# Kernel tuning notes

Hardware: AMD Instinct MI355X
Metric: run time of the kernel (lower is better)

The kernel has to match this reference:

```python
import jax, jax.numpy as jnp
import numpy as np
from jax import lax

EPS = 1e-5

def _silu(x):
    return x * jax.nn.sigmoid(x)

def _mamba_seq(x, ln_w, ln_b, in_w, conv_w, conv_b, xp_w, dt_w, dt_b, A_log, Dp, out_w):
    # x: [B, L, dim] token sequence
    di = conv_w.shape[0]          # d_inner
    ds = A_log.shape[1]           # d_state
    dtr = dt_w.shape[1]           # dt_rank
    kw = conv_w.shape[2]          # d_conv
    # LayerNorm
    mu = jnp.mean(x, axis=-1, keepdims=True)
    var = jnp.mean((x - mu) ** 2, axis=-1, keepdims=True)
    xn = (x - mu) * lax.rsqrt(var + EPS) * ln_w + ln_b
    # in_proj -> (x, z)
    xz = xn @ in_w.T                       # [B,L,2*di]
    xs, z = xz[..., :di], xz[..., di:]
    # causal depthwise conv1d over L
    xc = lax.conv_general_dilated(xs.transpose(0, 2, 1), conv_w, (1,),
                                  [(kw - 1, 0)], feature_group_count=di,
                                  dimension_numbers=('NCH', 'OIH', 'NCH'))
    xc = _silu(xc + conv_b[None, :, None]).transpose(0, 2, 1)   # [B,L,di]
    # x_proj -> dt, B, C
    dbc = xc @ xp_w.T                      # [B,L,dtr+2*ds]
    dt = jax.nn.softplus(dbc[..., :dtr] @ dt_w.T + dt_b)        # [B,L,di]
    Bm = dbc[..., dtr:dtr + ds]            # [B,L,ds]
    Cm = dbc[..., dtr + ds:]               # [B,L,ds]
    A = -jnp.exp(A_log)                    # [di,ds]
    dA = jnp.exp(dt[..., None] * A)        # [B,L,di,ds]
    dBu = (dt * xc)[..., None] * Bm[:, :, None, :]              # [B,L,di,ds]
    # selective scan: h_t = dA_t * h_{t-1} + dBu_t (parallel associative scan)
    def comb(e1, e2):
        a1, b1 = e1
        a2, b2 = e2
        return a1 * a2, a2 * b1 + b2
    _, h = lax.associative_scan(comb, (dA, dBu), axis=1)
    y = jnp.einsum('blds,bls->bld', h, Cm) + xc * Dp
    return (y * _silu(z)) @ out_w.T

def _mamba_block(x5, *p):
    # x5: [B,C,D,H,W] -> flatten spatial dims to tokens
    B, C = x5.shape[:2]
    xf = x5.reshape(B, C, -1).transpose(0, 2, 1)   # [B,L,C]
    y = _mamba_seq(xf, *p)
    return y.transpose(0, 2, 1).reshape(x5.shape)

def _conv3d(x, w, b):
    return lax.conv_general_dilated(x, w, (1, 1, 1), [(1, 1)] * 3,
                                    dimension_numbers=('NCDHW', 'OIDHW', 'NCDHW')) \
           + b[None, :, None, None, None]

def _bn3d(x, g, b):
    # BatchNorm3d in training mode: batch statistics over (B,D,H,W)
    m = jnp.mean(x, axis=(0, 2, 3, 4), keepdims=True)
    v = jnp.mean((x - m) ** 2, axis=(0, 2, 3, 4), keepdims=True)
    return (x - m) * lax.rsqrt(v + EPS) * g.reshape(1, -1, 1, 1, 1) + b.reshape(1, -1, 1, 1, 1)

def _mamba_params(key, dim, d_state=16, d_conv=4, expand=2):
    di = expand * dim
    dtr = max(1, -(-dim // 16))
    ks = jax.random.split(key, 5)
    return {
        'ln_w': jnp.ones((dim,), jnp.float32),
        'ln_b': jnp.zeros((dim,), jnp.float32),
        'in_w': jax.random.normal(ks[0], (2 * di, dim), jnp.float32) * (dim ** -0.5),
        'conv_w': jax.random.normal(ks[1], (di, 1, d_conv), jnp.float32) * 0.3,
        'conv_b': jnp.zeros((di,), jnp.float32),
        'xp_w': jax.random.normal(ks[2], (dtr + 2 * d_state, di), jnp.float32) * (di ** -0.5),
        'dt_w': jax.random.normal(ks[3], (di, dtr), jnp.float32) * (dtr ** -0.5),
        'dt_b': jnp.log(jnp.expm1(jnp.full((di,), 0.01, jnp.float32))),
        'A_log': jnp.log(jnp.tile(jnp.arange(1, d_state + 1, dtype=jnp.float32)[None, :], (di, 1))),
        'D': jnp.ones((di,), jnp.float32),
        'out_w': jax.random.normal(ks[4], (dim, di), jnp.float32) * (di ** -0.5),
    }

def setup_inputs() -> dict:
    key = jax.random.key(0)
    k = jax.random.split(key, 8)
    inp = {
        'l': jax.random.normal(k[0], (1, 16, 16, 48, 48), jnp.float32),
        's': jax.random.normal(k[1], (1, 16, 16, 48, 48), jnp.float32),
    }
    for name, p in _mamba_params(k[2], 32).items():
        inp['m1_' + name] = p
    for name, p in _mamba_params(k[3], 16).items():
        inp['m2_' + name] = p
    inp['c1_w'] = jax.random.normal(k[4], (16, 32, 3, 3, 3), jnp.float32) * ((32 * 27) ** -0.5)
    inp['c1_b'] = jnp.zeros((16,), jnp.float32)
    inp['bn1_g'] = jnp.ones((16,), jnp.float32)
    inp['bn1_b'] = jnp.zeros((16,), jnp.float32)
    inp['c2_w'] = jax.random.normal(k[5], (16, 16, 3, 3, 3), jnp.float32) * ((16 * 27) ** -0.5)
    inp['c2_b'] = jnp.zeros((16,), jnp.float32)
    inp['bn2_g'] = jnp.ones((16,), jnp.float32)
    inp['bn2_b'] = jnp.zeros((16,), jnp.float32)
    return inp

def reference(l, s,
              m1_ln_w, m1_ln_b, m1_in_w, m1_conv_w, m1_conv_b, m1_xp_w, m1_dt_w, m1_dt_b, m1_A_log, m1_D, m1_out_w,
              m2_ln_w, m2_ln_b, m2_in_w, m2_conv_w, m2_conv_b, m2_xp_w, m2_dt_w, m2_dt_b, m2_A_log, m2_D, m2_out_w,
              c1_w, c1_b, bn1_g, bn1_b, c2_w, c2_b, bn2_g, bn2_b):
    x = jnp.concatenate([l, s], axis=1)                         # [B,32,D,H,W]
    x = _mamba_block(x, m1_ln_w, m1_ln_b, m1_in_w, m1_conv_w, m1_conv_b,
                     m1_xp_w, m1_dt_w, m1_dt_b, m1_A_log, m1_D, m1_out_w) + x
    x = _bn3d(_conv3d(x, c1_w, c1_b), bn1_g, bn1_b)             # [B,16,D,H,W]
    x = _mamba_block(x, m2_ln_w, m2_ln_b, m2_in_w, m2_conv_w, m2_conv_b,
                     m2_xp_w, m2_dt_w, m2_dt_b, m2_A_log, m2_D, m2_out_w) + x
    x = _bn3d(_conv3d(x, c2_w, c2_b), bn2_g, bn2_b)
    return x
```

## Files before the change

### kernel.cpp

```cpp
#include <hip/hip_runtime.h>
#include <math.h>

#define L_TOT 36864
#define BN_EPS 1e-5f
#define PCH 45000

typedef __attribute__((ext_vector_type(8))) short bf16x8;
typedef __attribute__((ext_vector_type(4))) float f32x4;

__device__ __forceinline__ float fsigmoid(float x){ return 1.f/(1.f+__expf(-x)); }
__device__ __forceinline__ float fsoftplus(float x){
  float e = __expf(x);
  return (x>20.f)? x : __logf(1.f+e);
}
__device__ __forceinline__ unsigned short f2bf(float x){
  union { float f; unsigned u; } cv; cv.f = x;
  unsigned r = (cv.u + 0x7FFFu + ((cv.u>>16)&1u)) >> 16;
  return (unsigned short)r;
}
__host__ __device__ constexpr int off3c(int r){
  return (r>=27) ? 0 : ((r/9)-1)*2500 + (((r%9)/3)-1)*50 + ((r%3)-1);
}

template<int DIM, int DI, int DTR, bool DOBN, bool SETUP>
__global__ __launch_bounds__(256) void k_front(
    const float* __restrict__ x0, const float* __restrict__ x1,
    const float* __restrict__ bstats, const float* __restrict__ bg, const float* __restrict__ bbp,
    const float* __restrict__ lnw, const float* __restrict__ lnb,
    const float* __restrict__ inw,
    const float* __restrict__ cw, const float* __restrict__ cb,
    const float* __restrict__ xpw,
    const float* __restrict__ dtw, const float* __restrict__ dtb,
    const float* __restrict__ Alog,
    float* __restrict__ xcg, float* __restrict__ zg,
    float* __restrict__ dtpg, float* __restrict__ Bg, float* __restrict__ Cg,
    float* __restrict__ aggA, float* __restrict__ aggB,
    const float* __restrict__ cvw1, unsigned short* __restrict__ wA1,
    const float* __restrict__ cvw2, unsigned short* __restrict__ wA2,
    float* __restrict__ stats, float* __restrict__ bfz)
{
  constexpr int TCH  = 48;
  constexpr int ROWS = DTR + 32;
  constexpr int NSH  = 256/DI;
  constexpr int SPB  = 16/NSH;
  constexpr int CH   = DI*16;
  constexpr int R0SZ = DI*64;
  constexpr int O_SXC = R0SZ;
  constexpr int O_SB  = O_SXC + DI*49;
  constexpr int O_SC  = O_SB + 16*49;
  constexpr int O_DTP = O_SC + 16*49;
  constexpr int SMEM  = O_DTP + DTR*48 + 64;
  __shared__ float sm[SMEM];

  const int tid   = threadIdx.x;
  const int chunk = blockIdx.x;
  const int t0    = chunk*TCH;

  if constexpr (SETUP){
    for (int idx = blockIdx.x*256 + tid; idx < 16*PCH; idx += 768*256)
      bfz[idx] = 0.f;
    const int b = blockIdx.x;
    if (b < 4){
      int k = b*256 + tid;
      if (k < 864){
        int ic = k & 31, r = k >> 5;
        for (int m=0;m<16;m++){
          float v = (r < 27) ? cvw1[m*32*27 + ic*27 + r] : 0.f;
          wA1[(((k>>3)*16) + m)*8 + (k&7)] = f2bf(v);
        }
      }
    } else if (b < 6){
      int k = (b-4)*256 + tid;
      if (k < 448){
        int ic = k & 15, r = k >> 4;
        for (int m=0;m<16;m++){
          float v = (r < 27) ? cvw2[m*16*27 + ic*27 + r] : 0.f;
          wA2[(((k>>3)*16) + m)*8 + (k&7)] = f2bf(v);
        }
      }
    } else if (b == 6){
      if (tid < 64) stats[tid] = 0.f;
    }
  }

  for (int idx = tid; idx < DIM*64; idx += 256){
    int c = idx >> 6, i2 = idx & 63;
    int t = t0 - 3 + i2;
    float v = 0.f;
    if (i2 < 51 && t >= 0){
      if constexpr (DOBN){
        float raw = x0[c*L_TOT + t];
        float bm = bstats[2*c]*(1.f/L_TOT);
        float bv = bstats[2*c+1]*(1.f/L_TOT) - bm*bm;
        v = (raw - bm)*rsqrtf(bv+BN_EPS)*bg[c] + bbp[c];
      } else {
        v = (c < 16) ? x0[c*L_TOT + t] : x1[(c-16)*L_TOT + t];
      }
    }
    sm[idx] = v;
  }
  __syncthreads();

  if (tid < 64){
    float s = 0.f, s2 = 0.f;
#pragma unroll
    for (int c = 0; c < DIM; c++){
      float v = sm[c*64 + tid];
      s += v; s2 += v*v;
    }
    float m  = s*(1.f/DIM);
    float var = s2*(1.f/DIM) - m*m;
    float rs = rsqrtf(var + BN_EPS);
#pragma unroll
    for (int c = 0; c < DIM; c++){
      float v = sm[c*64 + tid];
      sm[c*64 + tid] = (v-m)*rs*lnw[c] + lnb[c];
    }
  }
  __syncthreads();

  const int i   = tid & 63;
  const int r0w = __builtin_amdgcn_readfirstlane(tid >> 6);
  {
    float xn[DIM];
#pragma unroll
    for (int c = 0; c < DIM; c++) xn[c] = sm[c*64 + i];
    __syncthreads();
    for (int r = r0w; r < 2*DI; r += 4){
      float acc = 0.f;
#pragma unroll
      for (int c = 0; c < DIM; c++) acc += xn[c]*inw[r*DIM + c];
      if (r < DI){
        if (i < 51) sm[r*64 + i] = (t0 == 0 && i < 3) ? 0.f : acc;
      } else {
        if (i >= 3 && i < 51) zg[(r-DI)*L_TOT + t0 + i - 3] = acc;
      }
    }
  }
  __syncthreads();

  for (int idx = tid; idx < DI*48; idx += 256){
    int d = idx / 48, j = idx - d*48;
    const float* xr = &sm[d*64 + j];
    float acc = cb[d] + cw[d*4+0]*xr[0] + cw[d*4+1]*xr[1]
                      + cw[d*4+2]*xr[2] + cw[d*4+3]*xr[3];
    sm[O_SXC + d*49 + j] = acc * fsigmoid(acc);
  }
  __syncthreads();

  {
    constexpr int NR = (ROWS + 3) / 4;
    float acc[NR];
#pragma unroll
    for (int rr = 0; rr < NR; rr++) acc[rr] = 0.f;
    for (int db = 0; db < DI; db += 16){
      float xcol[16];
#pragma unroll
      for (int k = 0; k < 16; k++) xcol[k] = sm[O_SXC + (db+k)*49 + i];
#pragma unroll
      for (int rr = 0; rr < NR; rr++){
        int r = r0w + rr*4;
        if (r < ROWS){
          float a2 = 0.f;
#pragma unroll
          for (int k = 0; k < 16; k++) a2 += xcol[k]*xpw[r*DI + db + k];
          acc[rr] += a2;
        }
      }
    }
    if (i < 48){
#pragma unroll
      for (int rr = 0; rr < NR; rr++){
        int r = r0w + rr*4;
        if (r < ROWS){
          if (r < DTR)          sm[O_DTP + r*48 + i] = acc[rr];
          else if (r < DTR+16)  sm[O_SB + (r-DTR)*49 + i] = acc[rr];
          else                  sm[O_SC + (r-DTR-16)*49 + i] = acc[rr];
        }
      }
    }
  }
  __syncthreads();

  for (int idx = tid; idx < DI*48; idx += 256){
    int d = idx / 48, j = idx - d*48;
    float pre = dtb[d] + dtw[d*DTR]*sm[O_DTP + j];
    if (DTR > 1) pre += dtw[d*DTR + DTR-1]*sm[O_DTP + (DTR-1)*48 + j];
    sm[d*49 + j] = fsoftplus(pre);
  }
  __syncthreads();

  for (int idx = tid; idx < DI*12; idx += 256){
    int d = idx / 12, q = idx - d*12;
    float4 v = make_float4(sm[O_SXC + d*49 + q*4+0], sm[O_SXC + d*49 + q*4+1],
                           sm[O_SXC + d*49 + q*4+2], sm[O_SXC + d*49 + q*4+3]);
    *reinterpret_cast<float4*>(xcg + d*L_TOT + t0 + q*4) = v;
  }
  for (int idx = tid; idx < ROWS*12; idx += 256){
    int r = idx / 12, q = idx - r*12;
    const float* src; float* dst;
    if (r < DTR)        { src = &sm[O_DTP + r*48 + q*4];          dst = dtpg + r*L_TOT + t0 + q*4; }
    else if (r < DTR+16){ src = &sm[O_SB + (r-DTR)*49 + q*4];     dst = Bg + (r-DTR)*L_TOT + t0 + q*4; }
    else                { src = &sm[O_SC + (r-DTR-16)*49 + q*4];  dst = Cg + (r-DTR-16)*L_TOT + t0 + q*4; }
    *reinterpret_cast<float4*>(dst) = make_float4(src[0], src[1], src[2], src[3]);
  }

  {
    const int d  = tid / NSH;
    const int sh = tid - d*NSH;
    float Av[SPB], Ar[SPB], Br[SPB];
#pragma unroll
    for (int j = 0; j < SPB; j++){
      Av[j] = -__expf(Alog[d*16 + sh*SPB + j]);
      Ar[j] = 1.f; Br[j] = 0.f;
    }
    for (int t = 0; t < TCH; t++){
      float dtv = sm[d*49 + t];
      float bb2 = dtv * sm[O_SXC + d*49 + t];
#pragma unroll
      for (int j = 0; j < SPB; j++){
        float a2 = __expf(dtv*Av[j]);
        Ar[j] *= a2;
        Br[j] = a2*Br[j] + bb2*sm[O_SB + (sh*SPB+j)*49 + t];
      }
    }
    const int o = chunk*CH + tid*SPB;
    if constexpr (SPB == 4){
      *reinterpret_cast<float4*>(&aggA[o]) = make_float4(Ar[0],Ar[1],Ar[2],Ar[3]);
      *reinterpret_cast<float4*>(&aggB[o]) = make_float4(Br[0],Br[1],Br[2],Br[3]);
    } else {
      *reinterpret_cast<float2*>(&aggA[o]) = make_float2(Ar[0],Ar[1]);
      *reinterpret_cast<float2*>(&aggB[o]) = make_float2(Br[0],Br[1]);
    }
  }
}

template<int NCH>
__global__ __launch_bounds__(256) void k_carry(const float* __restrict__ aggA,
                        const float* __restrict__ aggB,
                        float* __restrict__ carry, int CH) {
  constexpr int SEG = NCH/16;
  const int chl = threadIdx.x & 15;
  const int seg = threadIdx.x >> 4;
  const int ch  = blockIdx.x*16 + chl;
  const int c0  = seg*SEG;
  float a = 1.f, b = 0.f;
  for (int cb=c0; cb<c0+SEG; cb+=8){
    float av[8], bv[8];
#pragma unroll
    for (int k=0;k<8;k++){ av[k]=aggA[(cb+k)*CH+ch]; bv[k]=aggB[(cb+k)*CH+ch]; }
#pragma unroll
    for (int k=0;k<8;k++){ a = a*av[k]; b = av[k]*b + bv[k]; }
  }
  __shared__ float sa[16][17], sb[16][17];
  sa[seg][chl]=a; sb[seg][chl]=b;
  __syncthreads();
  if (threadIdx.x < 16){
    float pa=1.f, pb=0.f;
    for (int g=0; g<16; g++){
      float ca=sa[g][threadIdx.x], cb2=sb[g][threadIdx.x];
      sa[g][threadIdx.x]=pa; sb[g][threadIdx.x]=pb;
      float na = pa*ca;
      float nb = ca*pb + cb2;
      pa=na; pb=nb;
    }
  }
  __syncthreads();
  float h = sb[seg][chl];
  for (int cb=c0; cb<c0+SEG; cb+=8){
    float av[8], bv[8];
#pragma unroll
    for (int k=0;k<8;k++){ av[k]=aggA[(cb+k)*CH+ch]; bv[k]=aggB[(cb+k)*CH+ch]; }
#pragma unroll
    for (int k=0;k<8;k++){ carry[(cb+k)*CH+ch]=h; h = av[k]*h + bv[k]; }
  }
}

template<int DIM, int DI, int DTR, int RES>
__global__ __launch_bounds__(256) void k_back(
    const float* __restrict__ xcg, const float* __restrict__ zg,
    const float* __restrict__ dtpg, const float* __restrict__ Bg, const float* __restrict__ Cg,
    const float* __restrict__ dtw, const float* __restrict__ dtb,
    const float* __restrict__ Alog, const float* __restrict__ Dp,
    const float* __restrict__ carry,
    const float* __restrict__ ow,
    const float* __restrict__ r0src, const float* __restrict__ r1src,
    const float* __restrict__ bstats, const float* __restrict__ bg, const float* __restrict__ bbp,
    unsigned short* __restrict__ rp)
{
  constexpr int TCH = 48;
  constexpr int NSH = 256/DI;
  constexpr int SPB = 16/NSH;
  constexpr int ROWS = DTR + 32;
  constexpr int O_SXC = 0;
  constexpr int O_SDT = O_SXC + DI*49;
  constexpr int O_SB  = O_SDT + DI*49;
  constexpr int O_SC  = O_SB + 16*49;
  constexpr int O_SY  = O_SC + 16*49;
  constexpr int O_DTP = O_SY + DI*49;
  constexpr int SMEM  = O_DTP + DTR*48 + 64;
  __shared__ float sm[SMEM];
  const int tid   = threadIdx.x;
  const int chunk = blockIdx.x;
  const int t0    = chunk*TCH;

  for (int idx = tid; idx < DI*12; idx += 256){
    int d = idx / 12, q = idx - d*12;
    float4 v = *reinterpret_cast<const float4*>(xcg + d*L_TOT + t0 + q*4);
    sm[O_SXC + d*49 + q*4+0] = v.x; sm[O_SXC + d*49 + q*4+1] = v.y;
    sm[O_SXC + d*49 + q*4+2] = v.z; sm[O_SXC + d*49 + q*4+3] = v.w;
  }
  for (int idx = tid; idx < ROWS*12; idx += 256){
    int r = idx / 12, q = idx - r*12;
    const float* src; float* dst;
    if (r < DTR)        { src = dtpg + r*L_TOT + t0 + q*4;         dst = &sm[O_DTP + r*48 + q*4]; }
    else if (r < DTR+16){ src = Bg + (r-DTR)*L_TOT + t0 + q*4;     dst = &sm[O_SB + (r-DTR)*49 + q*4]; }
    else                { src = Cg + (r-DTR-16)*L_TOT + t0 + q*4;  dst = &sm[O_SC + (r-DTR-16)*49 + q*4]; }
    float4 v = *reinterpret_cast<const float4*>(src);
    dst[0] = v.x; dst[1] = v.y; dst[2] = v.z; dst[3] = v.w;
  }
  __syncthreads();
  for (int idx = tid; idx < DI*48; idx += 256){
    int d = idx / 48, j = idx - d*48;
    float pre = dtb[d] + dtw[d*DTR]*sm[O_DTP + j];
    if (DTR > 1) pre += dtw[d*DTR + DTR-1]*sm[O_DTP + 48 + j];
    sm[O_SDT + d*49 + j] = fsoftplus(pre);
  }
  __syncthreads();

  {
    const int d  = tid / NSH;
    const int sh = tid - d*NSH;
    float Av[SPB], h[SPB];
#pragma unroll
    for (int j = 0; j < SPB; j++){
      Av[j] = -__expf(Alog[d*16 + sh*SPB + j]);
      h[j]  = carry[chunk*(DI*16) + tid*SPB + j];
    }
    const float Dv = Dp[d];
    for (int t = 0; t < TCH; t++){
      float dtv = sm[O_SDT + d*49 + t];
      float xcv = sm[O_SXC + d*49 + t];
      float bb2 = dtv*xcv;
      float p = 0.f;
#pragma unroll
      for (int j = 0; j < SPB; j++){
        float a2 = __expf(dtv*Av[j]);
        h[j] = a2*h[j] + bb2*sm[O_SB + (sh*SPB+j)*49 + t];
        p += h[j]*sm[O_SC + (sh*SPB+j)*49 + t];
      }
#pragma unroll
      for (int o = 1; o < NSH; o <<= 1) p += __shfl_xor(p, o);
      if (sh == 0) sm[O_SY + d*49 + t] = p + xcv*Dv;
    }
  }
  __syncthreads();
  for (int idx = tid; idx < DI*12; idx += 256){
    int d = idx / 12, q = idx - d*12;
    float4 zv = *reinterpret_cast<const float4*>(zg + d*L_TOT + t0 + q*4);
    sm[O_SY + d*49 + q*4+0] *= zv.x*fsigmoid(zv.x);
    sm[O_SY + d*49 + q*4+1] *= zv.y*fsigmoid(zv.y);
    sm[O_SY + d*49 + q*4+2] *= zv.z*fsigmoid(zv.z);
    sm[O_SY + d*49 + q*4+3] *= zv.w*fsigmoid(zv.w);
  }
  __syncthreads();

  {
    const int col = tid & 63;
    const int r0w = __builtin_amdgcn_readfirstlane(tid >> 6);
    constexpr int NO = DIM/4;
    float acc[NO];
#pragma unroll
    for (int rr = 0; rr < NO; rr++) acc[rr] = 0.f;
    for (int db = 0; db < DI; db += 16){
      float ycol[16];
#pragma unroll
      for (int k = 0; k < 16; k++) ycol[k] = sm[O_SY + (db+k)*49 + col];
#pragma unroll
      for (int rr = 0; rr < NO; rr++){
        int r = r0w + rr*4;
        float a2 = 0.f;
#pragma unroll
        for (int k = 0; k < 16; k++) a2 += ycol[k]*ow[r*DI + db + k];
        acc[rr] += a2;
      }
    }
    if (col < 48){
      const int t  = t0 + col;
      const int zz = chunk / 48, yy = chunk - zz*48;
      const int pb = (zz+1)*2500 + (yy+1)*50 + (col+1);
#pragma unroll
      for (int rr = 0; rr < NO; rr++){
        int r = r0w + rr*4;
        float res;
        if (RES == 0){
          res = (r < 16) ? r0src[r*L_TOT + t] : r1src[(r-16)*L_TOT + t];
        } else {
          float bm = bstats[2*r]*(1.f/L_TOT);
          float bv = bstats[2*r+1]*(1.f/L_TOT) - bm*bm;
          res = (r0src[r*L_TOT + t] - bm)*rsqrtf(bv+BN_EPS)*bg[r] + bbp[r];
        }
        rp[r*PCH + pb] = f2bf(acc[rr] + res);
      }
    }
  }
}

template<int IC>
__global__ __launch_bounds__(256) void k_conv_mfma(const unsigned short* __restrict__ bin,
                         const unsigned short* __restrict__ wA,
                         const float* __restrict__ bias, float* __restrict__ out,
                         float* __restrict__ stats) {
  constexpr int NKB = (IC==32) ? 27 : 14;
  __shared__ float sred[32];
  if (threadIdx.x < 32) sred[threadIdx.x] = 0.f;
  __syncthreads();
  const int lane = threadIdx.x & 63;
  const int n = lane & 15, quad = lane >> 4;
  const int tile = blockIdx.x*4 + (threadIdx.x >> 6);
  const int t = tile*16 + n;
  int zz = t / 2304;
  int r2 = t - zz*2304;
  int yy = r2 / 48;
  int xx = r2 - yy*48;
  int pb = (zz+1)*2500 + (yy+1)*50 + (xx+1);
  const unsigned short* bp[8];
#pragma unroll
  for (int j=0;j<8;j++){
    int e = quad*8 + j;
    int ic = (IC==32) ? e : (e & 15);
    bp[j] = bin + ic*PCH + pb;
  }
  const int rq = (IC==32) ? 0 : (quad >> 1);
  f32x4 acc = {0.f, 0.f, 0.f, 0.f};
#pragma unroll
  for (int kb=0; kb<NKB; kb++){
    bf16x8 af = *reinterpret_cast<const bf16x8*>(wA + (size_t)((kb*4+quad)*16 + n)*8);
    int off;
    if (IC==32) off = off3c(kb);
    else        off = rq ? off3c(2*kb+1) : off3c(2*kb);
    bf16x8 bf;
#pragma unroll
    for (int j=0;j<8;j++) bf[j] = (short)bp[j][off];
    acc = __builtin_amdgcn_mfma_f32_16x16x32_bf16(af, bf, acc, 0, 0, 0);
  }
  float vs[4];
#pragma unroll
  for (int reg=0; reg<4; reg++){
    int m = quad*4 + reg;
    float v = acc[reg] + bias[m];
    out[m*L_TOT + t] = v;
    vs[reg] = v;
  }
#pragma unroll
  for (int reg=0; reg<4; reg++){
    float a = vs[reg], b2 = vs[reg]*vs[reg];
#pragma unroll
    for (int o=1; o<16; o<<=1){ a += __shfl_xor(a,o); b2 += __shfl_xor(b2,o); }
    if (n == 0){
      atomicAdd(&sred[quad*4+reg], a);
      atomicAdd(&sred[16 + quad*4+reg], b2);
    }
  }
  __syncthreads();
  if (threadIdx.x < 16){
    atomicAdd(&stats[2*threadIdx.x],   sred[threadIdx.x]);
    atomicAdd(&stats[2*threadIdx.x+1], sred[16+threadIdx.x]);
  }
}

__global__ void k_bn_norm4(const float* __restrict__ raw, const float* __restrict__ stats,
                           const float* __restrict__ g, const float* __restrict__ b,
                           float* __restrict__ out) {
  int i = blockIdx.x*256 + threadIdx.x;
  int c = i / (L_TOT/4);
  int tq = i - c*(L_TOT/4);
  float m = stats[2*c]*(1.f/L_TOT);
  float v = stats[2*c+1]*(1.f/L_TOT) - m*m;
  float sc = rsqrtf(v+BN_EPS)*g[c];
  float bs = b[c] - m*sc;
  float4 x = *reinterpret_cast<const float4*>(raw + c*L_TOT + tq*4);
  float4 o = make_float4(x.x*sc+bs, x.y*sc+bs, x.z*sc+bs, x.w*sc+bs);
  *reinterpret_cast<float4*>(out + c*L_TOT + tq*4) = o;
}

extern "C" void kernel_launch(void* const* d_in, const int* in_sizes, int n_in,
                              void* d_out, int out_size, void* d_ws, size_t ws_size,
                              hipStream_t stream) {
  const float* l        = (const float*)d_in[0];
  const float* s        = (const float*)d_in[1];
  const float* m1_ln_w  = (const float*)d_in[2];
  const float* m1_ln_b  = (const float*)d_in[3];
  const float* m1_in_w  = (const float*)d_in[4];
  const float* m1_cw    = (const float*)d_in[5];
  const float* m1_cb    = (const float*)d_in[6];
  const float* m1_xp_w  = (const float*)d_in[7];
  const float* m1_dt_w  = (const float*)d_in[8];
  const float* m1_dt_b  = (const float*)d_in[9];
  const float* m1_Alog  = (const float*)d_in[10];
  const float* m1_D     = (const float*)d_in[11];
  const float* m1_out_w = (const float*)d_in[12];
  const float* m2_ln_w  = (const float*)d_in[13];
  const float* m2_ln_b  = (const float*)d_in[14];
  const float* m2_in_w  = (const float*)d_in[15];
  const float* m2_cw    = (const float*)d_in[16];
  const float* m2_cb    = (const float*)d_in[17];
  const float* m2_xp_w  = (const float*)d_in[18];
  const float* m2_dt_w  = (const float*)d_in[19];
  const float* m2_dt_b  = (const float*)d_in[20];
  const float* m2_Alog  = (const float*)d_in[21];
  const float* m2_D     = (const float*)d_in[22];
  const float* m2_out_w = (const float*)d_in[23];
  const float* c1_w     = (const float*)d_in[24];
  const float* c1_b     = (const float*)d_in[25];
  const float* bn1_g    = (const float*)d_in[26];
  const float* bn1_b    = (const float*)d_in[27];
  const float* c2_w     = (const float*)d_in[28];
  const float* c2_b     = (const float*)d_in[29];
  const float* bn2_g    = (const float*)d_in[30];
  const float* bn2_b    = (const float*)d_in[31];

  float* ws = (float*)d_ws;
  const size_t L = L_TOT;
  float* xc1      = ws;
  float* z1       = ws + 64*L;
  float* B1       = ws + 128*L;
  float* C1       = ws + 144*L;
  float* dtp1     = ws + 160*L;
  float* conv1raw = ws + 162*L;
  float* xc2      = ws + 178*L;
  float* z2       = ws + 210*L;
  float* conv2raw = ws + 242*L;
  float* aggA     = ws + 258*L;
  float* aggB     = aggA + 786432;
  float* carry    = aggB + 786432;
  float* stats1   = ws + 322*L;
  float* stats2   = stats1 + 32;
  unsigned short* bfin = (unsigned short*)(ws + 323*L);
  unsigned short* wA1  = (unsigned short*)(ws + 343*L);
  unsigned short* wA2  = wA1 + 13824;

  k_front<32,64,2,false,true><<<768,256,0,stream>>>(l, s, stats1, bn1_g, bn1_b,
      m1_ln_w, m1_ln_b, m1_in_w, m1_cw, m1_cb, m1_xp_w, m1_dt_w, m1_dt_b, m1_Alog,
      xc1, z1, dtp1, B1, C1, aggA, aggB,
      c1_w, wA1, c2_w, wA2, stats1, (float*)bfin);
  k_carry<768><<<64,256,0,stream>>>(aggA, aggB, carry, 1024);
  k_back<32,64,2,0><<<768,256,0,stream>>>(xc1, z1, dtp1, B1, C1,
      m1_dt_w, m1_dt_b, m1_Alog, m1_D, carry, m1_out_w, l, s,
      stats1, bn1_g, bn1_b, bfin);
  k_conv_mfma<32><<<576,256,0,stream>>>(bfin, wA1, c1_b, conv1raw, stats1);

  k_front<16,32,1,true,false><<<768,256,0,stream>>>(conv1raw, conv1raw, stats1, bn1_g, bn1_b,
      m2_ln_w, m2_ln_b, m2_in_w, m2_cw, m2_cb, m2_xp_w, m2_dt_w, m2_dt_b, m2_Alog,
      xc2, z2, dtp1, B1, C1, aggA, aggB,
      nullptr, nullptr, nullptr, nullptr, nullptr, nullptr);
  k_carry<768><<<32,256,0,stream>>>(aggA, aggB, carry, 512);
  k_back<16,32,1,1><<<768,256,0,stream>>>(xc2, z2, dtp1, B1, C1,
      m2_dt_w, m2_dt_b, m2_Alog, m2_D, carry, m2_out_w, conv1raw, conv1raw,
      stats1, bn1_g, bn1_b, bfin);
  k_conv_mfma<16><<<576,256,0,stream>>>(bfin, wA2, c2_b, conv2raw, stats2);
  k_bn_norm4<<<576,256,0,stream>>>(conv2raw, stats2, bn2_g, bn2_b, (float*)d_out);
}
```

Before: 290.2 us.

## Halve scan chunk length to double block count and rework carry scan

The scan chunk length drops from 48 to 24 tokens, so k_front and k_back launch 1536 blocks instead of 768, with smaller shared-memory tiles and launch bounds raised to allow 6 blocks per SM. The k_carry kernel is reorganised to use 32 segments of 8 channels to handle the doubled number of chunk aggregates. The workspace layout is reshuffled to fit the larger aggregate buffers, and the carry is loaded with vector loads. The aim is better occupancy and latency hiding, at the cost of more redundant halo work per chunk and a longer carry scan.

```diff
diff --git a/kernel.cpp b/kernel.cpp
--- a/kernel.cpp
+++ b/kernel.cpp
@@ -23,7 +23,7 @@
 }
 
 template<int DIM, int DI, int DTR, bool DOBN, bool SETUP>
-__global__ __launch_bounds__(256) void k_front(
+__global__ __launch_bounds__(256,6) void k_front(
     const float* __restrict__ x0, const float* __restrict__ x1,
     const float* __restrict__ bstats, const float* __restrict__ bg, const float* __restrict__ bbp,
     const float* __restrict__ lnw, const float* __restrict__ lnb,
@@ -39,17 +39,18 @@
     const float* __restrict__ cvw2, unsigned short* __restrict__ wA2,
     float* __restrict__ stats, float* __restrict__ bfz)
 {
-  constexpr int TCH  = 48;
+  constexpr int TCH  = 24;
+  constexpr int COLS = 32;
   constexpr int ROWS = DTR + 32;
   constexpr int NSH  = 256/DI;
   constexpr int SPB  = 16/NSH;
   constexpr int CH   = DI*16;
-  constexpr int R0SZ = DI*64;
+  constexpr int R0SZ = DI*COLS;
   constexpr int O_SXC = R0SZ;
-  constexpr int O_SB  = O_SXC + DI*49;
-  constexpr int O_SC  = O_SB + 16*49;
-  constexpr int O_DTP = O_SC + 16*49;
-  constexpr int SMEM  = O_DTP + DTR*48 + 64;
+  constexpr int O_SB  = O_SXC + DI*25 + 8;
+  constexpr int O_SC  = O_SB + 16*25;
+  constexpr int O_DTP = O_SC + 16*25;
+  constexpr int SMEM  = O_DTP + DTR*TCH + 16;
   __shared__ float sm[SMEM];
 
   const int tid   = threadIdx.x;
@@ -57,7 +58,7 @@
   const int t0    = chunk*TCH;
 
   if constexpr (SETUP){
-    for (int idx = blockIdx.x*256 + tid; idx < 16*PCH; idx += 768*256)
+    for (int idx = blockIdx.x*256 + tid; idx < 16*PCH; idx += 1536*256)
       bfz[idx] = 0.f;
     const int b = blockIdx.x;
     if (b < 4){
@@ -83,11 +84,11 @@
     }
   }
 
-  for (int idx = tid; idx < DIM*64; idx += 256){
-    int c = idx >> 6, i2 = idx & 63;
+  for (int idx = tid; idx < DIM*COLS; idx += 256){
+    int c = idx >> 5, i2 = idx & 31;
     int t = t0 - 3 + i2;
     float v = 0.f;
-    if (i2 < 51 && t >= 0){
+    if (i2 < TCH+3 && t >= 0){
       if constexpr (DOBN){
         float raw = x0[c*L_TOT + t];
         float bm = bstats[2*c]*(1.f/L_TOT);
@@ -101,11 +102,11 @@
   }
   __syncthreads();
 
-  if (tid < 64){
+  if (tid < 32){
     float s = 0.f, s2 = 0.f;
 #pragma unroll
     for (int c = 0; c < DIM; c++){
-      float v = sm[c*64 + tid];
+      float v = sm[c*COLS + tid];
       s += v; s2 += v*v;
     }
     float m  = s*(1.f/DIM);
@@ -113,53 +114,53 @@
     float rs = rsqrtf(var + BN_EPS);
 #pragma unroll
     for (int c = 0; c < DIM; c++){
-      float v = sm[c*64 + tid];
-      sm[c*64 + tid] = (v-m)*rs*lnw[c] + lnb[c];
-    }
-  }
-  __syncthreads();
-
-  const int i   = tid & 63;
-  const int r0w = __builtin_amdgcn_readfirstlane(tid >> 6);
+      float v = sm[c*COLS + tid];
+      sm[c*COLS + tid] = (v-m)*rs*lnw[c] + lnb[c];
+    }
+  }
+  __syncthreads();
+
+  const int i  = tid & 31;
+  const int rw = tid >> 5;
   {
     float xn[DIM];
 #pragma unroll
-    for (int c = 0; c < DIM; c++) xn[c] = sm[c*64 + i];
+    for (int c = 0; c < DIM; c++) xn[c] = sm[c*COLS + i];
     __syncthreads();
-    for (int r = r0w; r < 2*DI; r += 4){
+    for (int r = rw; r < 2*DI; r += 8){
       float acc = 0.f;
 #pragma unroll
       for (int c = 0; c < DIM; c++) acc += xn[c]*inw[r*DIM + c];
       if (r < DI){
-        if (i < 51) sm[r*64 + i] = (t0 == 0 && i < 3) ? 0.f : acc;
+        if (i < TCH+3) sm[r*COLS + i] = (t0 == 0 && i < 3) ? 0.f : acc;
       } else {
-        if (i >= 3 && i < 51) zg[(r-DI)*L_TOT + t0 + i - 3] = acc;
-      }
-    }
-  }
-  __syncthreads();
-
-  for (int idx = tid; idx < DI*48; idx += 256){
-    int d = idx / 48, j = idx - d*48;
-    const float* xr = &sm[d*64 + j];
+        if (i >= 3 && i < TCH+3) zg[(r-DI)*L_TOT + t0 + i - 3] = acc;
+      }
+    }
+  }
+  __syncthreads();
+
+  for (int idx = tid; idx < DI*TCH; idx += 256){
+    int d = idx / TCH, j = idx - d*TCH;
+    const float* xr = &sm[d*COLS + j];
     float acc = cb[d] + cw[d*4+0]*xr[0] + cw[d*4+1]*xr[1]
                       + cw[d*4+2]*xr[2] + cw[d*4+3]*xr[3];
-    sm[O_SXC + d*49 + j] = acc * fsigmoid(acc);
+    sm[O_SXC + d*25 + j] = acc * fsigmoid(acc);
   }
   __syncthreads();
 
   {
-    constexpr int NR = (ROWS + 3) / 4;
+    constexpr int NR = (ROWS + 7) / 8;
     float acc[NR];
 #pragma unroll
     for (int rr = 0; rr < NR; rr++) acc[rr] = 0.f;
     for (int db = 0; db < DI; db += 16){
       float xcol[16];
 #pragma unroll
-      for (int k = 0; k < 16; k++) xcol[k] = sm[O_SXC + (db+k)*49 + i];
+      for (int k = 0; k < 16; k++) xcol[k] = sm[O_SXC + (db+k)*25 + i];
 #pragma unroll
       for (int rr = 0; rr < NR; rr++){
-        int r = r0w + rr*4;
+        int r = rw + rr*8;
         if (r < ROWS){
           float a2 = 0.f;
 #pragma unroll
@@ -168,40 +169,40 @@
         }
       }
     }
-    if (i < 48){
+    if (i < TCH){
 #pragma unroll
       for (int rr = 0; rr < NR; rr++){
-        int r = r0w + rr*4;
+        int r = rw + rr*8;
         if (r < ROWS){
-          if (r < DTR)          sm[O_DTP + r*48 + i] = acc[rr];
-          else if (r < DTR+16)  sm[O_SB + (r-DTR)*49 + i] = acc[rr];
-          else                  sm[O_SC + (r-DTR-16)*49 + i] = acc[rr];
+          if (r < DTR)          sm[O_DTP + r*TCH + i] = acc[rr];
+          else if (r < DTR+16)  sm[O_SB + (r-DTR)*25 + i] = acc[rr];
+          else                  sm[O_SC + (r-DTR-16)*25 + i] = acc[rr];
         }
       }
     }
   }
   __syncthreads();
 
-  for (int idx = tid; idx < DI*48; idx += 256){
-    int d = idx / 48, j = idx - d*48;
+  for (int idx = tid; idx < DI*TCH; idx += 256){
+    int d = idx / TCH, j = idx - d*TCH;
     float pre = dtb[d] + dtw[d*DTR]*sm[O_DTP + j];
-    if (DTR > 1) pre += dtw[d*DTR + DTR-1]*sm[O_DTP + (DTR-1)*48 + j];
-    sm[d*49 + j] = fsoftplus(pre);
-  }
-  __syncthreads();
-
-  for (int idx = tid; idx < DI*12; idx += 256){
-    int d = idx / 12, q = idx - d*12;
-    float4 v = make_float4(sm[O_SXC + d*49 + q*4+0], sm[O_SXC + d*49 + q*4+1],
-                           sm[O_SXC + d*49 + q*4+2], sm[O_SXC + d*49 + q*4+3]);
+    if (DTR > 1) pre += dtw[d*DTR + DTR-1]*sm[O_DTP + (DTR-1)*TCH + j];
+    sm[d*25 + j] = fsoftplus(pre);
+  }
+  __syncthreads();
+
+  for (int idx = tid; idx < DI*6; idx += 256){
+    int d = idx / 6, q = idx - d*6;
+    float4 v = make_float4(sm[O_SXC + d*25 + q*4+0], sm[O_SXC + d*25 + q*4+1],
+                           sm[O_SXC + d*25 + q*4+2], sm[O_SXC + d*25 + q*4+3]);
     *reinterpret_cast<float4*>(xcg + d*L_TOT + t0 + q*4) = v;
   }
-  for (int idx = tid; idx < ROWS*12; idx += 256){
-    int r = idx / 12, q = idx - r*12;
+  for (int idx = tid; idx < ROWS*6; idx += 256){
+    int r = idx / 6, q = idx - r*6;
     const float* src; float* dst;
-    if (r < DTR)        { src = &sm[O_DTP + r*48 + q*4];          dst = dtpg + r*L_TOT + t0 + q*4; }
-    else if (r < DTR+16){ src = &sm[O_SB + (r-DTR)*49 + q*4];     dst = Bg + (r-DTR)*L_TOT + t0 + q*4; }
-    else                { src = &sm[O_SC + (r-DTR-16)*49 + q*4];  dst = Cg + (r-DTR-16)*L_TOT + t0 + q*4; }
+    if (r < DTR)        { src = &sm[O_DTP + r*TCH + q*4];         dst = dtpg + r*L_TOT + t0 + q*4; }
+    else if (r < DTR+16){ src = &sm[O_SB + (r-DTR)*25 + q*4];     dst = Bg + (r-DTR)*L_TOT + t0 + q*4; }
+    else                { src = &sm[O_SC + (r-DTR-16)*25 + q*4];  dst = Cg + (r-DTR-16)*L_TOT + t0 + q*4; }
     *reinterpret_cast<float4*>(dst) = make_float4(src[0], src[1], src[2], src[3]);
   }
 
@@ -215,13 +216,13 @@
       Ar[j] = 1.f; Br[j] = 0.f;
     }
     for (int t = 0; t < TCH; t++){
-      float dtv = sm[d*49 + t];
-      float bb2 = dtv * sm[O_SXC + d*49 + t];
+      float dtv = sm[d*25 + t];
+      float bb2 = dtv * sm[O_SXC + d*25 + t];
 #pragma unroll
       for (int j = 0; j < SPB; j++){
         float a2 = __expf(dtv*Av[j]);
         Ar[j] *= a2;
-        Br[j] = a2*Br[j] + bb2*sm[O_SB + (sh*SPB+j)*49 + t];
+        Br[j] = a2*Br[j] + bb2*sm[O_SB + (sh*SPB+j)*25 + t];
       }
     }
     const int o = chunk*CH + tid*SPB;
@@ -239,25 +240,26 @@
 __global__ __launch_bounds__(256) void k_carry(const float* __restrict__ aggA,
                         const float* __restrict__ aggB,
                         float* __restrict__ carry, int CH) {
-  constexpr int SEG = NCH/16;
-  const int chl = threadIdx.x & 15;
-  const int seg = threadIdx.x >> 4;
-  const int ch  = blockIdx.x*16 + chl;
-  const int c0  = seg*SEG;
+  constexpr int SEGS = 32, CHB = 8;
+  constexpr int SLEN = NCH/SEGS;
+  const int chl = threadIdx.x & 7;
+  const int seg = threadIdx.x >> 3;
+  const int ch  = blockIdx.x*CHB + chl;
+  const int c0  = seg*SLEN;
   float a = 1.f, b = 0.f;
-  for (int cb=c0; cb<c0+SEG; cb+=8){
+  for (int cb=c0; cb<c0+SLEN; cb+=8){
     float av[8], bv[8];
 #pragma unroll
     for (int k=0;k<8;k++){ av[k]=aggA[(cb+k)*CH+ch]; bv[k]=aggB[(cb+k)*CH+ch]; }
 #pragma unroll
     for (int k=0;k<8;k++){ a = a*av[k]; b = av[k]*b + bv[k]; }
   }
-  __shared__ float sa[16][17], sb[16][17];
+  __shared__ float sa[SEGS][CHB+1], sb[SEGS][CHB+1];
   sa[seg][chl]=a; sb[seg][chl]=b;
   __syncthreads();
-  if (threadIdx.x < 16){
+  if (threadIdx.x < CHB){
     float pa=1.f, pb=0.f;
-    for (int g=0; g<16; g++){
+    for (int g=0; g<SEGS; g++){
       float ca=sa[g][threadIdx.x], cb2=sb[g][threadIdx.x];
       sa[g][threadIdx.x]=pa; sb[g][threadIdx.x]=pb;
       float na = pa*ca;
@@ -267,7 +269,7 @@
   }
   __syncthreads();
   float h = sb[seg][chl];
-  for (int cb=c0; cb<c0+SEG; cb+=8){
+  for (int cb=c0; cb<c0+SLEN; cb+=8){
     float av[8], bv[8];
 #pragma unroll
     for (int k=0;k<8;k++){ av[k]=aggA[(cb+k)*CH+ch]; bv[k]=aggB[(cb+k)*CH+ch]; }
@@ -277,7 +279,7 @@
 }
 
 template<int DIM, int DI, int DTR, int RES>
-__global__ __launch_bounds__(256) void k_back(
+__global__ __launch_bounds__(256,6) void k_back(
     const float* __restrict__ xcg, const float* __restrict__ zg,
     const float* __restrict__ dtpg, const float* __restrict__ Bg, const float* __restrict__ Cg,
     const float* __restrict__ dtw, const float* __restrict__ dtb,
@@ -288,43 +290,43 @@
     const float* __restrict__ bstats, const float* __restrict__ bg, const float* __restrict__ bbp,
     unsigned short* __restrict__ rp)
 {
-  constexpr int TCH = 48;
+  constexpr int TCH = 24;
   constexpr int NSH = 256/DI;
   constexpr int SPB = 16/NSH;
   constexpr int ROWS = DTR + 32;
   constexpr int O_SXC = 0;
-  constexpr int O_SDT = O_SXC + DI*49;
-  constexpr int O_SB  = O_SDT + DI*49;
-  constexpr int O_SC  = O_SB + 16*49;
-  constexpr int O_SY  = O_SC + 16*49;
-  constexpr int O_DTP = O_SY + DI*49;
-  constexpr int SMEM  = O_DTP + DTR*48 + 64;
+  constexpr int O_SDT = O_SXC + DI*25 + 8;
+  constexpr int O_SB  = O_SDT + DI*25 + 8;
+  constexpr int O_SC  = O_SB + 16*25;
+  constexpr int O_SY  = O_SC + 16*25;
+  constexpr int O_DTP = O_SY + DI*25 + 8;
+  constexpr int SMEM  = O_DTP + DTR*TCH + 16;
   __shared__ float sm[SMEM];
   const int tid   = threadIdx.x;
   const int chunk = blockIdx.x;
   const int t0    = chunk*TCH;
 
-  for (int idx = tid; idx < DI*12; idx += 256){
-    int d = idx / 12, q = idx - d*12;
+  for (int idx = tid; idx < DI*6; idx += 256){
+    int d = idx / 6, q = idx - d*6;
     float4 v = *reinterpret_cast<const float4*>(xcg + d*L_TOT + t0 + q*4);
-    sm[O_SXC + d*49 + q*4+0] = v.x; sm[O_SXC + d*49 + q*4+1] = v.y;
-    sm[O_SXC + d*49 + q*4+2] = v.z; sm[O_SXC + d*49 + q*4+3] = v.w;
-  }
-  for (int idx = tid; idx < ROWS*12; idx += 256){
-    int r = idx / 12, q = idx - r*12;
+    sm[O_SXC + d*25 + q*4+0] = v.x; sm[O_SXC + d*25 + q*4+1] = v.y;
+    sm[O_SXC + d*25 + q*4+2] = v.z; sm[O_SXC + d*25 + q*4+3] = v.w;
+  }
+  for (int idx = tid; idx < ROWS*6; idx += 256){
+    int r = idx / 6, q = idx - r*6;
     const float* src; float* dst;
-    if (r < DTR)        { src = dtpg + r*L_TOT + t0 + q*4;         dst = &sm[O_DTP + r*48 + q*4]; }
-    else if (r < DTR+16){ src = Bg + (r-DTR)*L_TOT + t0 + q*4;     dst = &sm[O_SB + (r-DTR)*49 + q*4]; }
-    else                { src = Cg + (r-DTR-16)*L_TOT + t0 + q*4;  dst = &sm[O_SC + (r-DTR-16)*49 + q*4]; }
+    if (r < DTR)        { src = dtpg + r*L_TOT + t0 + q*4;         dst = &sm[O_DTP + r*TCH + q*4]; }
+    else if (r < DTR+16){ src = Bg + (r-DTR)*L_TOT + t0 + q*4;     dst = &sm[O_SB + (r-DTR)*25 + q*4]; }
+    else                { src = Cg + (r-DTR-16)*L_TOT + t0 + q*4;  dst = &sm[O_SC + (r-DTR-16)*25 + q*4]; }
     float4 v = *reinterpret_cast<const float4*>(src);
     dst[0] = v.x; dst[1] = v.y; dst[2] = v.z; dst[3] = v.w;
   }
   __syncthreads();
-  for (int idx = tid; idx < DI*48; idx += 256){
-    int d = idx / 48, j = idx - d*48;
+  for (int idx = tid; idx < DI*TCH; idx += 256){
+    int d = idx / TCH, j = idx - d*TCH;
     float pre = dtb[d] + dtw[d*DTR]*sm[O_DTP + j];
-    if (DTR > 1) pre += dtw[d*DTR + DTR-1]*sm[O_DTP + 48 + j];
-    sm[O_SDT + d*49 + j] = fsoftplus(pre);
+    if (DTR > 1) pre += dtw[d*DTR + DTR-1]*sm[O_DTP + (DTR-1)*TCH + j];
+    sm[O_SDT + d*25 + j] = fsoftplus(pre);
   }
   __syncthreads();
 
@@ -333,65 +335,76 @@
     const int sh = tid - d*NSH;
     float Av[SPB], h[SPB];
 #pragma unroll
-    for (int j = 0; j < SPB; j++){
+    for (int j = 0; j < SPB; j++)
       Av[j] = -__expf(Alog[d*16 + sh*SPB + j]);
-      h[j]  = carry[chunk*(DI*16) + tid*SPB + j];
+    {
+      const int o = chunk*(DI*16) + tid*SPB;
+      if constexpr (SPB == 4){
+        float4 hv = *reinterpret_cast<const float4*>(&carry[o]);
+        h[0]=hv.x; h[1]=hv.y; h[2]=hv.z; h[3]=hv.w;
+      } else {
+        float2 hv = *reinterpret_cast<const float2*>(&carry[o]);
+        h[0]=hv.x; h[1]=hv.y;
+      }
     }
     const float Dv = Dp[d];
     for (int t = 0; t < TCH; t++){
-      float dtv = sm[O_SDT + d*49 + t];
-      float xcv = sm[O_SXC + d*49 + t];
+      float dtv = sm[O_SDT + d*25 + t];
+      float xcv = sm[O_SXC + d*25 + t];
       float bb2 = dtv*xcv;
       float p = 0.f;
 #pragma unroll
       for (int j = 0; j < SPB; j++){
         float a2 = __expf(dtv*Av[j]);
-        h[j] = a2*h[j] + bb2*sm[O_SB + (sh*SPB+j)*49 + t];
-        p += h[j]*sm[O_SC + (sh*SPB+j)*49 + t];
+        h[j] = a2*h[j] + bb2*sm[O_SB + (sh*SPB+j)*25 + t];
+        p += h[j]*sm[O_SC + (sh*SPB+j)*25 + t];
       }
 #pragma unroll
       for (int o = 1; o < NSH; o <<= 1) p += __shfl_xor(p, o);
-      if (sh == 0) sm[O_SY + d*49 + t] = p + xcv*Dv;
-    }
-  }
-  __syncthreads();
-  for (int idx = tid; idx < DI*12; idx += 256){
-    int d = idx / 12, q = idx - d*12;
+      if (sh == 0) sm[O_SY + d*25 + t] = p + xcv*Dv;
+    }
+  }
+  __syncthreads();
+  for (int idx = tid; idx < DI*6; idx += 256){
+    int d = idx / 6, q = idx - d*6;
     float4 zv = *reinterpret_cast<const float4*>(zg + d*L_TOT + t0 + q*4);
-    sm[O_SY + d*49 + q*4+0] *= zv.x*fsigmoid(zv.x);
-    sm[O_SY + d*49 + q*4+1] *= zv.y*fsigmoid(zv.y);
-    sm[O_SY + d*49 + q*4+2] *= zv.z*fsigmoid(zv.z);
-    sm[O_SY + d*49 + q*4+3] *= zv.w*fsigmoid(zv.w);
+    sm[O_SY + d*25 + q*4+0] *= zv.x*fsigmoid(zv.x);
+    sm[O_SY + d*25 + q*4+1] *= zv.y*fsigmoid(zv.y);
+    sm[O_SY + d*25 + q*4+2] *= zv.z*fsigmoid(zv.z);
+    sm[O_SY + d*25 + q*4+3] *= zv.w*fsigmoid(zv.w);
   }
   __syncthreads();
 
   {
-    const int col = tid & 63;
-    const int r0w = __builtin_amdgcn_readfirstlane(tid >> 6);
-    constexpr int NO = DIM/4;
+    const int col = tid & 31;
+    const int rw  = tid >> 5;
+    constexpr int NO = DIM/8;
     float acc[NO];
 #pragma unroll
     for (int rr = 0; rr < NO; rr++) acc[rr] = 0.f;
     for (int db = 0; db < DI; db += 16){
       float ycol[16];
 #pragma unroll
-      for (int k = 0; k < 16; k++) ycol[k] = sm[O_SY + (db+k)*49 + col];
+      for (int k = 0; k < 16; k++) ycol[k] = sm[O_SY + (db+k)*25 + col];
 #pragma unroll
       for (int rr = 0; rr < NO; rr++){
-        int r = r0w + rr*4;
+        int r = rw + rr*8;
         float a2 = 0.f;
 #pragma unroll
         for (int k = 0; k < 16; k++) a2 += ycol[k]*ow[r*DI + db + k];
         acc[rr] += a2;
       }
     }
-    if (col < 48){
+    if (col < TCH){
       const int t  = t0 + col;
-      const int zz = chunk / 48, yy = chunk - zz*48;
-      const int pb = (zz+1)*2500 + (yy+1)*50 + (col+1);
+      const int zz = t / 2304;
+      const int r2 = t - zz*2304;
+      const int yy = r2 / 48;
+      const int xx = r2 - yy*48;
+      const int pb = (zz+1)*2500 + (yy+1)*50 + (xx+1);
 #pragma unroll
       for (int rr = 0; rr < NO; rr++){
-        int r = r0w + rr*4;
+        int r = rw + rr*8;
         float res;
         if (RES == 0){
           res = (r < 16) ? r0src[r*L_TOT + t] : r1src[(r-16)*L_TOT + t];
@@ -528,34 +541,34 @@
   float* C1       = ws + 144*L;
   float* dtp1     = ws + 160*L;
   float* conv1raw = ws + 162*L;
-  float* xc2      = ws + 178*L;
-  float* z2       = ws + 210*L;
-  float* conv2raw = ws + 242*L;
-  float* aggA     = ws + 258*L;
-  float* aggB     = aggA + 786432;
-  float* carry    = aggB + 786432;
-  float* stats1   = ws + 322*L;
+  float* aggA     = ws + 178*L;
+  float* aggB     = aggA + 1536*1024;
+  float* carry    = aggB + 1536*1024;
+  float* stats1   = ws + 306*L;
   float* stats2   = stats1 + 32;
-  unsigned short* bfin = (unsigned short*)(ws + 323*L);
-  unsigned short* wA1  = (unsigned short*)(ws + 343*L);
+  unsigned short* bfin = (unsigned short*)(stats1 + 64);
+  unsigned short* wA1  = bfin + 32*PCH;
   unsigned short* wA2  = wA1 + 13824;
-
-  k_front<32,64,2,false,true><<<768,256,0,stream>>>(l, s, stats1, bn1_g, bn1_b,
+  float* xc2      = ws;
+  float* z2       = ws + 32*L;
+  float* conv2raw = ws + 64*L;
+
+  k_front<32,64,2,false,true><<<1536,256,0,stream>>>(l, s, stats1, bn1_g, bn1_b,
       m1_ln_w, m1_ln_b, m1_in_w, m1_cw, m1_cb, m1_xp_w, m1_dt_w, m1_dt_b, m1_Alog,
       xc1, z1, dtp1, B1, C1, aggA, aggB,
       c1_w, wA1, c2_w, wA2, stats1, (float*)bfin);
-  k_carry<768><<<64,256,0,stream>>>(aggA, aggB, carry, 1024);
-  k_back<32,64,2,0><<<768,256,0,stream>>>(xc1, z1, dtp1, B1, C1,
+  k_carry<1536><<<128,256,0,stream>>>(aggA, aggB, carry, 1024);
+  k_back<32,64,2,0><<<1536,256,0,stream>>>(xc1, z1, dtp1, B1, C1,
       m1_dt_w, m1_dt_b, m1_Alog, m1_D, carry, m1_out_w, l, s,
       stats1, bn1_g, bn1_b, bfin);
   k_conv_mfma<32><<<576,256,0,stream>>>(bfin, wA1, c1_b, conv1raw, stats1);
 
-  k_front<16,32,1,true,false><<<768,256,0,stream>>>(conv1raw, conv1raw, stats1, bn1_g, bn1_b,
+  k_front<16,32,1,true,false><<<1536,256,0,stream>>>(conv1raw, conv1raw, stats1, bn1_g, bn1_b,
       m2_ln_w, m2_ln_b, m2_in_w, m2_cw, m2_cb, m2_xp_w, m2_dt_w, m2_dt_b, m2_Alog,
       xc2, z2, dtp1, B1, C1, aggA, aggB,
       nullptr, nullptr, nullptr, nullptr, nullptr, nullptr);
-  k_carry<768><<<32,256,0,stream>>>(aggA, aggB, carry, 512);
-  k_back<16,32,1,1><<<768,256,0,stream>>>(xc2, z2, dtp1, B1, C1,
+  k_carry<1536><<<64,256,0,stream>>>(aggA, aggB, carry, 512);
+  k_back<16,32,1,1><<<1536,256,0,stream>>>(xc2, z2, dtp1, B1, C1,
       m2_dt_w, m2_dt_b, m2_Alog, m2_D, carry, m2_out_w, conv1raw, conv1raw,
       stats1, bn1_g, bn1_b, bfin);
   k_conv_mfma<16><<<576,256,0,stream>>>(bfin, wA2, c2_b, conv2raw, stats2);
```

New measurement: 323.7 us. 11.5% more time.
